# Kernel optimization log

Hardware: AMD Instinct MI355X
Metric: run time of the kernel (lower is better)

## Reference

```python
import jax, jax.numpy as jnp
import numpy as np

B, S, D, V = 4, 2048, 512, 32000
MAVG_BETA = 0.9  # effective beta (cache_update_steps >= warm_mvavg_steps)
EPS = 1e-12


def _l2norm(v):
    # matches torch F.normalize(p=2, dim=-1, eps=1e-12)
    n = jnp.maximum(jnp.linalg.norm(v, axis=-1, keepdims=True), EPS)
    return v / n


def setup_inputs() -> dict:
    key = jax.random.key(0)
    k1, k2, k3, k4 = jax.random.split(key, 4)
    x = jax.random.normal(k1, (B, S, D), dtype=jnp.float32)
    p = jax.random.uniform(k2, (B, S, V), dtype=jnp.float32)
    gold = jax.random.randint(k3, (B, S), 0, V, dtype=jnp.int64)
    gold_pad_mask = jnp.zeros((B, S), dtype=bool)
    cache_p = jax.random.normal(k4, (V, D), dtype=jnp.float32) * 0.02
    return {"x": x, "p": p, "gold": gold, "gold_pad_mask": gold_pad_mask, "cache_p": cache_p}


def reference(x, p, gold, gold_pad_mask, cache_p):
    # ---- loss: masked sum MSE between L2-normalized x and gathered cache rows ----
    c_p = _l2norm(cache_p[gold])              # [B,S,D] gather
    xn = _l2norm(x)
    keep = (~gold_pad_mask).astype(x.dtype)[..., None]
    loss = jnp.sum(((xn - c_p) ** 2) * keep)

    # ---- cache update: gather p at gold, weight x, segment-mean by gold id ----
    p_gold = jnp.take_along_axis(p, gold[..., None], axis=-1)   # [B,S,1]
    contrib = jnp.where(gold_pad_mask[..., None], 0.0, x * p_gold)
    flat_gold = gold.reshape(-1)                                 # [B*S]
    sums = jax.ops.segment_sum(contrib.reshape(-1, x.shape[-1]), flat_gold, num_segments=cache_p.shape[0])
    counts = jax.ops.segment_sum(jnp.ones_like(flat_gold, dtype=x.dtype), flat_gold, num_segments=cache_p.shape[0])
    avg = sums / jnp.maximum(counts, 1.0)[:, None]
    blended = MAVG_BETA * cache_p + (1.0 - MAVG_BETA) * avg
    new_cache_p = jnp.where((counts > 0)[:, None], blended, cache_p)
    return loss, new_cache_p
```

## Files before the change

### kernel.cpp

```cpp
#include <hip/hip_runtime.h>
#include <hip/hip_bf16.h>

#define BD 4
#define SD 2048
#define DD 512
#define VD 32000
#define NTOK (BD * SD)
#define EPS_L2 1e-12f
#define RPB 16
#define NBLK (VD / RPB)
#define MAXTOK 32

typedef float f32x4u __attribute__((ext_vector_type(4), aligned(4)));


__global__ void __launch_bounds__(1024, 2)
fused_row_kernel(const float* __restrict__ x, const float* __restrict__ p,
                 const int* __restrict__ gold, const int* __restrict__ mask,
                 const float* __restrict__ cache, float* __restrict__ out,
                 float* __restrict__ lossSlot) {
    __shared__ int lcnt[RPB];
    __shared__ int ltok[RPB][MAXTOK];
    __shared__ float lpw[RPB][MAXTOK];
    __shared__ float lossW[RPB];

    int tid = threadIdx.x;
    int base = blockIdx.x * RPB;
    if (tid < RPB) lcnt[tid] = 0;
    __syncthreads();

    #pragma unroll
    for (int k = 0; k < NTOK / 1024; ++k) {
        int i = tid + k * 1024;
        int g = gold[i];
        unsigned r = (unsigned)(g - base);
        if (r < (unsigned)RPB) {
            int slot = atomicAdd(&lcnt[r], 1);
            if (slot < MAXTOK) {
                ltok[r][slot] = i;
                float pg = p[(size_t)i * VD + g];
                lpw[r][slot] = mask[i] ? -1.f : pg;
            }
        }
    }
    __syncthreads();

    int w = tid >> 6;
    int lane = tid & 63;
    int row = base + w;
    int b = lane * 4;
    const float4* cr = (const float4*)cache + (size_t)row * (DD / 4);
    float4 ca = cr[lane], cb = cr[64 + lane];
    float* o = out + 1 + (size_t)row * DD;
    int cnt = lcnt[w];

    float lossAcc = 0.f;
    float4 va, vb;
    if (cnt == 0) {
        va = ca;
        vb = cb;
    } else {
        float sc = ca.x * ca.x + ca.y * ca.y + ca.z * ca.z + ca.w * ca.w
                 + cb.x * cb.x + cb.y * cb.y + cb.z * cb.z + cb.w * cb.w;
        #pragma unroll
        for (int off = 32; off; off >>= 1) sc += __shfl_xor(sc, off, 64);
        float rnc = 1.0f / fmaxf(sqrtf(sc), EPS_L2);

        float4 aa = {0.f, 0.f, 0.f, 0.f}, ab = {0.f, 0.f, 0.f, 0.f};
        for (int k = 0; k < cnt; ++k) {
            int t = ltok[w][k];
            float pw = lpw[w][k];
            const float4* xr = (const float4*)x + (size_t)t * (DD / 4);
            float4 xa = xr[lane], xb = xr[64 + lane];

            float dot = xa.x * ca.x + xa.y * ca.y + xa.z * ca.z + xa.w * ca.w
                      + xb.x * cb.x + xb.y * cb.y + xb.z * cb.z + xb.w * cb.w;
            float sx = xa.x * xa.x + xa.y * xa.y + xa.z * xa.z + xa.w * xa.w
                     + xb.x * xb.x + xb.y * xb.y + xb.z * xb.z + xb.w * xb.w;
            #pragma unroll
            for (int off = 32; off; off >>= 1) {
                dot += __shfl_xor(dot, off, 64);
                sx += __shfl_xor(sx, off, 64);
            }
            if (pw >= 0.f) {
                float rnx = 1.0f / fmaxf(sqrtf(sx), EPS_L2);
                lossAcc += 2.f - 2.f * dot * rnx * rnc;
                aa.x += pw * xa.x; aa.y += pw * xa.y;
                aa.z += pw * xa.z; aa.w += pw * xa.w;
                ab.x += pw * xb.x; ab.y += pw * xb.y;
                ab.z += pw * xb.z; ab.w += pw * xb.w;
            }
        }
        float m = 0.1f / (float)cnt;
        va.x = 0.9f * ca.x + m * aa.x; va.y = 0.9f * ca.y + m * aa.y;
        va.z = 0.9f * ca.z + m * aa.z; va.w = 0.9f * ca.w + m * aa.w;
        vb.x = 0.9f * cb.x + m * ab.x; vb.y = 0.9f * cb.y + m * ab.y;
        vb.z = 0.9f * cb.z + m * ab.z; vb.w = 0.9f * cb.w + m * ab.w;
    }
    f32x4u sva = {va.x, va.y, va.z, va.w};
    f32x4u svb = {vb.x, vb.y, vb.z, vb.w};
    *(f32x4u*)(o + b) = sva;
    *(f32x4u*)(o + 256 + b) = svb;

    if (lane == 0) lossW[w] = lossAcc;
    __syncthreads();
    if (tid == 0) {
        float s = 0.f;
        #pragma unroll
        for (int j = 0; j < RPB; ++j) s += lossW[j];
        lossSlot[blockIdx.x] = s;
    }
}

__global__ void __launch_bounds__(256)
loss_reduce_kernel(const float* __restrict__ lossSlot, float* __restrict__ out) {
    __shared__ float sm[4];
    float a = 0.f;
    for (int i = threadIdx.x; i < NBLK; i += 256) a += lossSlot[i];
    #pragma unroll
    for (int off = 32; off; off >>= 1) a += __shfl_xor(a, off, 64);
    if ((threadIdx.x & 63) == 0) sm[threadIdx.x >> 6] = a;
    __syncthreads();
    if (threadIdx.x == 0) out[0] = sm[0] + sm[1] + sm[2] + sm[3];
}

extern "C" void kernel_launch(void* const* d_in, const int* in_sizes, int n_in,
                              void* d_out, int out_size, void* d_ws, size_t ws_size,
                              hipStream_t stream) {
    const float* x = (const float*)d_in[0];
    const float* p = (const float*)d_in[1];
    const int* gold = (const int*)d_in[2];
    const int* mask = (const int*)d_in[3];
    const float* cache = (const float*)d_in[4];
    float* out = (float*)d_out;
    float* lossSlot = (float*)d_ws;

    fused_row_kernel<<<NBLK, 1024, 0, stream>>>(x, p, gold, mask, cache, out,
                                                lossSlot);
    loss_reduce_kernel<<<1, 256, 0, stream>>>(lossSlot, out);
}
```

Baseline: 35.03 us.

## Process 64 cache rows per block with vectorized gold scan and prefetch

Each block now owns 64 vocabulary rows instead of 16, with each wave looping over 4 rows. This cuts the number of blocks that must each rescan the whole gold array by a factor of four. The gold scan reads int4 vectors, and the first cache row is loaded before the scan to overlap its latency. The token loop is also clamped to MAXTOK. The trade-off is fewer blocks and more serial work per wave, which may reduce parallelism across the GPU.

```diff
diff --git a/kernel.cpp b/kernel.cpp
--- a/kernel.cpp
+++ b/kernel.cpp
@@ -7,7 +7,7 @@
 #define VD 32000
 #define NTOK (BD * SD)
 #define EPS_L2 1e-12f
-#define RPB 16
+#define RPB 64
 #define NBLK (VD / RPB)
 #define MAXTOK 32
 
@@ -22,92 +22,111 @@
     __shared__ int lcnt[RPB];
     __shared__ int ltok[RPB][MAXTOK];
     __shared__ float lpw[RPB][MAXTOK];
-    __shared__ float lossW[RPB];
+    __shared__ float lossW[16];
 
     int tid = threadIdx.x;
     int base = blockIdx.x * RPB;
     if (tid < RPB) lcnt[tid] = 0;
     __syncthreads();
 
+    int w = tid >> 6;
+    int lane = tid & 63;
+    int row0 = base + w * 4;
+    int b = lane * 4;
+
+    const float4* cr0 = (const float4*)cache + (size_t)row0 * (DD / 4);
+    float4 pca = cr0[lane], pcb = cr0[64 + lane];
+
+    const int4* g4 = (const int4*)gold;
     #pragma unroll
-    for (int k = 0; k < NTOK / 1024; ++k) {
-        int i = tid + k * 1024;
-        int g = gold[i];
-        unsigned r = (unsigned)(g - base);
-        if (r < (unsigned)RPB) {
-            int slot = atomicAdd(&lcnt[r], 1);
-            if (slot < MAXTOK) {
-                ltok[r][slot] = i;
-                float pg = p[(size_t)i * VD + g];
-                lpw[r][slot] = mask[i] ? -1.f : pg;
+    for (int k = 0; k < NTOK / 4096; ++k) {
+        int idx = tid + k * 1024;
+        int4 gg = g4[idx];
+        int gi[4] = {gg.x, gg.y, gg.z, gg.w};
+        #pragma unroll
+        for (int c = 0; c < 4; ++c) {
+            unsigned r = (unsigned)(gi[c] - base);
+            if (r < (unsigned)RPB) {
+                int i = idx * 4 + c;
+                int slot = atomicAdd(&lcnt[r], 1);
+                if (slot < MAXTOK) {
+                    ltok[r][slot] = i;
+                    float pg = p[(size_t)i * VD + gi[c]];
+                    lpw[r][slot] = mask[i] ? -1.f : pg;
+                }
             }
         }
     }
     __syncthreads();
 
-    int w = tid >> 6;
-    int lane = tid & 63;
-    int row = base + w;
-    int b = lane * 4;
-    const float4* cr = (const float4*)cache + (size_t)row * (DD / 4);
-    float4 ca = cr[lane], cb = cr[64 + lane];
-    float* o = out + 1 + (size_t)row * DD;
-    int cnt = lcnt[w];
+    float lossAcc = 0.f;
+    #pragma unroll
+    for (int rr = 0; rr < 4; ++rr) {
+        int row = row0 + rr;
+        float4 ca, cb;
+        if (rr == 0) { ca = pca; cb = pcb; }
+        else {
+            const float4* cr = (const float4*)cache + (size_t)row * (DD / 4);
+            ca = cr[lane]; cb = cr[64 + lane];
+        }
+        float* o = out + 1 + (size_t)row * DD;
+        int rb = w * 4 + rr;
+        int cnt = lcnt[rb];
 
-    float lossAcc = 0.f;
-    float4 va, vb;
-    if (cnt == 0) {
-        va = ca;
-        vb = cb;
-    } else {
-        float sc = ca.x * ca.x + ca.y * ca.y + ca.z * ca.z + ca.w * ca.w
-                 + cb.x * cb.x + cb.y * cb.y + cb.z * cb.z + cb.w * cb.w;
-        #pragma unroll
-        for (int off = 32; off; off >>= 1) sc += __shfl_xor(sc, off, 64);
-        float rnc = 1.0f / fmaxf(sqrtf(sc), EPS_L2);
+        float4 va, vb;
+        if (cnt == 0) {
+            va = ca; vb = cb;
+        } else {
+            float sc = ca.x * ca.x + ca.y * ca.y + ca.z * ca.z + ca.w * ca.w
+                     + cb.x * cb.x + cb.y * cb.y + cb.z * cb.z + cb.w * cb.w;
+            #pragma unroll
+            for (int off = 32; off; off >>= 1) sc += __shfl_xor(sc, off, 64);
+            float rnc = 1.0f / fmaxf(sqrtf(sc), EPS_L2);
 
-        float4 aa = {0.f, 0.f, 0.f, 0.f}, ab = {0.f, 0.f, 0.f, 0.f};
-        for (int k = 0; k < cnt; ++k) {
-            int t = ltok[w][k];
-            float pw = lpw[w][k];
-            const float4* xr = (const float4*)x + (size_t)t * (DD / 4);
-            float4 xa = xr[lane], xb = xr[64 + lane];
+            float4 aa = {0.f, 0.f, 0.f, 0.f}, ab = {0.f, 0.f, 0.f, 0.f};
+            int kend = cnt < MAXTOK ? cnt : MAXTOK;
+            for (int k = 0; k < kend; ++k) {
+                int t = ltok[rb][k];
+                float pw = lpw[rb][k];
+                const float4* xr = (const float4*)x + (size_t)t * (DD / 4);
+                float4 xa = xr[lane], xb = xr[64 + lane];
 
-            float dot = xa.x * ca.x + xa.y * ca.y + xa.z * ca.z + xa.w * ca.w
-                      + xb.x * cb.x + xb.y * cb.y + xb.z * cb.z + xb.w * cb.w;
-            float sx = xa.x * xa.x + xa.y * xa.y + xa.z * xa.z + xa.w * xa.w
-                     + xb.x * xb.x + xb.y * xb.y + xb.z * xb.z + xb.w * xb.w;
-            #pragma unroll
-            for (int off = 32; off; off >>= 1) {
-                dot += __shfl_xor(dot, off, 64);
-                sx += __shfl_xor(sx, off, 64);
+                float dot = xa.x * ca.x + xa.y * ca.y + xa.z * ca.z + xa.w * ca.w
+                          + xb.x * cb.x + xb.y * cb.y + xb.z * cb.z + xb.w * cb.w;
+                float sx = xa.x * xa.x + xa.y * xa.y + xa.z * xa.z + xa.w * xa.w
+                         + xb.x * xb.x + xb.y * xb.y + xb.z * xb.z + xb.w * xb.w;
+                #pragma unroll
+                for (int off = 32; off; off >>= 1) {
+                    dot += __shfl_xor(dot, off, 64);
+                    sx += __shfl_xor(sx, off, 64);
+                }
+                if (pw >= 0.f) {
+                    float rnx = 1.0f / fmaxf(sqrtf(sx), EPS_L2);
+                    lossAcc += 2.f - 2.f * dot * rnx * rnc;
+                    aa.x += pw * xa.x; aa.y += pw * xa.y;
+                    aa.z += pw * xa.z; aa.w += pw * xa.w;
+                    ab.x += pw * xb.x; ab.y += pw * xb.y;
+                    ab.z += pw * xb.z; ab.w += pw * xb.w;
+                }
             }
-            if (pw >= 0.f) {
-                float rnx = 1.0f / fmaxf(sqrtf(sx), EPS_L2);
-                lossAcc += 2.f - 2.f * dot * rnx * rnc;
-                aa.x += pw * xa.x; aa.y += pw * xa.y;
-                aa.z += pw * xa.z; aa.w += pw * xa.w;
-                ab.x += pw * xb.x; ab.y += pw * xb.y;
-                ab.z += pw * xb.z; ab.w += pw * xb.w;
-            }
+            float m = 0.1f / (float)cnt;
+            va.x = 0.9f * ca.x + m * aa.x; va.y = 0.9f * ca.y + m * aa.y;
+            va.z = 0.9f * ca.z + m * aa.z; va.w = 0.9f * ca.w + m * aa.w;
+            vb.x = 0.9f * cb.x + m * ab.x; vb.y = 0.9f * cb.y + m * ab.y;
+            vb.z = 0.9f * cb.z + m * ab.z; vb.w = 0.9f * cb.w + m * ab.w;
         }
-        float m = 0.1f / (float)cnt;
-        va.x = 0.9f * ca.x + m * aa.x; va.y = 0.9f * ca.y + m * aa.y;
-        va.z = 0.9f * ca.z + m * aa.z; va.w = 0.9f * ca.w + m * aa.w;
-        vb.x = 0.9f * cb.x + m * ab.x; vb.y = 0.9f * cb.y + m * ab.y;
-        vb.z = 0.9f * cb.z + m * ab.z; vb.w = 0.9f * cb.w + m * ab.w;
+        f32x4u sva = {va.x, va.y, va.z, va.w};
+        f32x4u svb = {vb.x, vb.y, vb.z, vb.w};
+        *(f32x4u*)(o + b) = sva;
+        *(f32x4u*)(o + 256 + b) = svb;
     }
-    f32x4u sva = {va.x, va.y, va.z, va.w};
-    f32x4u svb = {vb.x, vb.y, vb.z, vb.w};
-    *(f32x4u*)(o + b) = sva;
-    *(f32x4u*)(o + 256 + b) = svb;
 
     if (lane == 0) lossW[w] = lossAcc;
     __syncthreads();
     if (tid == 0) {
         float s = 0.f;
         #pragma unroll
-        for (int j = 0; j < RPB; ++j) s += lossW[j];
+        for (int j = 0; j < 16; ++j) s += lossW[j];
         lossSlot[blockIdx.x] = s;
     }
 }
```

New measurement: 34.38 us. No clear change (-1.9%).
